# Kernel optimization log

Hardware: AMD Instinct MI355X
Metric: run time of the kernel (lower is better)

Reference implementation:

```python
import jax, jax.numpy as jnp
import numpy as np

D = 8       # q_dim / embed dim
NF = 8      # num_feats
OUT = 8     # out_dim


def _get_emb(sin_inp):
    # interleaved sin/cos, matching positional_encodings.get_emb
    return jnp.stack([jnp.sin(sin_inp), jnp.cos(sin_inp)], axis=-1).reshape(sin_inp.shape[0], -1)


def pos_encoding_2d(X, Y, ch, dtype=jnp.float32):
    # PositionalEncoding2D over dims (X=window, Y=num_feats), channels=ch
    c = int(np.ceil(ch / 4) * 2)
    inv_freq = jnp.asarray((1.0 / (10000.0 ** (np.arange(0, c, 2) / np.float32(c)))).astype(np.float32))
    emb_x = _get_emb(jnp.arange(X, dtype=dtype)[:, None] * inv_freq[None, :])  # (X, c)
    emb_y = _get_emb(jnp.arange(Y, dtype=dtype)[:, None] * inv_freq[None, :])  # (Y, c)
    emb = jnp.zeros((X, Y, 2 * c), dtype)
    emb = emb.at[:, :, :c].set(emb_x[:, None, :])
    emb = emb.at[:, :, c:2 * c].set(emb_y[None, :, :])
    return emb[:, :, :ch]


def layer_norm(x, g, b, eps=1e-5):
    mu = jnp.mean(x, axis=-1, keepdims=True)
    var = jnp.mean((x - mu) ** 2, axis=-1, keepdims=True)
    return (x - mu) * jax.lax.rsqrt(var + eps) * g + b


def setup_inputs() -> dict:
    key = jax.random.key(0)
    ks = jax.random.split(key, 12)
    B, W = 128, 2048
    x = jax.random.normal(ks[0], (B, W, NF), dtype=jnp.float32)
    m = jax.random.randint(ks[1], (B, W, NF), 0, 2, dtype=jnp.int32)
    m = m.at[:, :, 0].set(0)  # guarantee at least one unmasked key per row
    s = 0.1
    return {
        "x": x,
        "m": m,
        "emb_w": jax.random.normal(ks[2], (D, 1), jnp.float32) * s,
        "emb_b": jax.random.normal(ks[3], (D,), jnp.float32) * s,
        "emb_ln_g": jnp.ones((D,), jnp.float32),
        "emb_ln_b": jnp.zeros((D,), jnp.float32),
        "ln_g": jnp.ones((D,), jnp.float32),
        "ln_b": jnp.zeros((D,), jnp.float32),
        "var_query": jax.random.normal(ks[4], (1, 1, D), jnp.float32) * s,
        "in_proj_w": jax.random.normal(ks[5], (3 * D, D), jnp.float32) * s,
        "in_proj_b": jax.random.normal(ks[6], (3 * D,), jnp.float32) * s,
        "out_proj_w": jax.random.normal(ks[7], (D, D), jnp.float32) * s,
        "out_proj_b": jax.random.normal(ks[8], (D,), jnp.float32) * s,
        "proj_w": jax.random.normal(ks[9], (OUT, D), jnp.float32) * s,
        "proj_b": jax.random.normal(ks[10], (OUT,), jnp.float32) * s,
    }


def reference(x, m, emb_w, emb_b, emb_ln_g, emb_ln_b, ln_g, ln_b, var_query,
              in_proj_w, in_proj_b, out_proj_w, out_proj_b, proj_w, proj_b):
    B, W, F = x.shape
    d = emb_w.shape[0]
    # LinearEmbed: Linear(1, d) on each scalar, then LayerNorm(d)
    h = x[..., None] * emb_w[:, 0] + emb_b              # (B, W, F, d)
    h = layer_norm(h, emb_ln_g, emb_ln_b)
    # 2D positional encoding over (window, feature) dims
    h = h + pos_encoding_2d(W, F, d)[None]
    # pre-attention LayerNorm
    h = layer_norm(h, ln_g, ln_b)
    # single-query multihead (1 head) cross attention, key_padding_mask = m
    Wq, Wk, Wv = in_proj_w[:d], in_proj_w[d:2 * d], in_proj_w[2 * d:]
    bq, bk, bv = in_proj_b[:d], in_proj_b[d:2 * d], in_proj_b[2 * d:]
    qv = Wq @ var_query.reshape(d) + bq                 # (d,) shared query
    k = jnp.einsum('bwfd,ed->bwfe', h, Wk) + bk         # (B, W, F, d)
    v = jnp.einsum('bwfd,ed->bwfe', h, Wv) + bv         # (B, W, F, d)
    logits = jnp.einsum('bwfe,e->bwf', k, qv) / jnp.sqrt(jnp.float32(d))
    logits = jnp.where(m.astype(bool), -jnp.inf, logits)
    attn_w = jax.nn.softmax(logits, axis=-1)            # (B, W, F)
    attn = jnp.einsum('bwf,bwfe->bwe', attn_w, v)       # (B, W, d)
    attn = attn @ out_proj_w.T + out_proj_b
    # final projection
    out = attn @ proj_w.T + proj_b                      # (B, W, OUT)
    return out
```

## Files before the change

### kernel.cpp

```cpp
#include <hip/hip_runtime.h>
#include <math.h>

#define THREADS 256
#define W_DIM 2048
#define INV_SQRT8 0.35355339059327373f

__global__ __launch_bounds__(THREADS) void misstsm_fused(
    const float* __restrict__ x, const int* __restrict__ m,
    const float* __restrict__ emb_w, const float* __restrict__ emb_b,
    const float* __restrict__ emb_ln_g, const float* __restrict__ emb_ln_b,
    const float* __restrict__ ln_g, const float* __restrict__ ln_b,
    const float* __restrict__ var_query,
    const float* __restrict__ in_proj_w, const float* __restrict__ in_proj_b,
    const float* __restrict__ out_proj_w, const float* __restrict__ out_proj_b,
    const float* __restrict__ proj_w, const float* __restrict__ proj_b,
    float* __restrict__ out, int npos)
{
    __shared__ float s_M2[64];
    __shared__ float s_c2[8];
    __shared__ float s_a[8], s_bb[8], s_wlg[8];
    __shared__ float s_F[8][9];
    __shared__ float s_sc[12];

    const int t = threadIdx.x;
    const int half = npos >> 1;
    const int pos = blockIdx.x * THREADS + t;
    const int lp  = (pos < half) ? pos : (half - 1);

    const float4* xv4 = reinterpret_cast<const float4*>(x);
    const int4*   mv4 = reinterpret_cast<const int4*>(m);
    const float4 xa0 = xv4[lp*2+0],        xb0 = xv4[lp*2+1];
    const float4 xa1 = xv4[(lp+half)*2+0], xb1 = xv4[(lp+half)*2+1];
    const int4   ma0 = mv4[lp*2+0],        mb0 = mv4[lp*2+1];
    const int4   ma1 = mv4[(lp+half)*2+0], mb1 = mv4[(lp+half)*2+1];

    if (t < 64) {
        const int p = t >> 3, d = t & 7;
        float acc = 0.0f;
        #pragma unroll
        for (int e = 0; e < 8; ++e) {
            float po = 0.0f;
            #pragma unroll
            for (int o = 0; o < 8; ++o) po = fmaf(proj_w[p*8+o], out_proj_w[o*8+e], po);
            acc = fmaf(po, in_proj_w[(16+e)*8 + d], acc);
        }
        s_M2[t] = acc * ln_g[d];
    } else if (t < 72) {
        const int d = t - 64;
        float wk = 0.0f;
        #pragma unroll
        for (int e = 0; e < 8; ++e) {
            float qe = in_proj_b[e];
            #pragma unroll
            for (int dd = 0; dd < 8; ++dd) qe = fmaf(in_proj_w[e*8+dd], var_query[dd], qe);
            wk = fmaf(in_proj_w[(8+e)*8 + d], qe, wk);
        }
        s_wlg[d] = ln_g[d] * wk * INV_SQRT8;
    } else if (t < 80) {
        const int d = t - 72;
        float ewm = 0.0f, ebm = 0.0f;
        #pragma unroll
        for (int dd = 0; dd < 8; ++dd) { ewm += emb_w[dd]; ebm += emb_b[dd]; }
        ewm *= 0.125f; ebm *= 0.125f;
        s_a[d]  = (emb_w[d] - ewm) * emb_ln_g[d];
        s_bb[d] = (emb_b[d] - ebm) * emb_ln_g[d];
    } else if (t == 80) {
        float ewm = 0.0f, ebm = 0.0f;
        #pragma unroll
        for (int d = 0; d < 8; ++d) { ewm += emb_w[d]; ebm += emb_b[d]; }
        ewm *= 0.125f; ebm *= 0.125f;
        float A = 0.0f, Bc = 0.0f, Cc = 0.0f;
        #pragma unroll
        for (int d = 0; d < 8; ++d) {
            const float dw = emb_w[d] - ewm, db = emb_b[d] - ebm;
            A = fmaf(dw, dw, A); Bc = fmaf(dw, db, Bc); Cc = fmaf(db, db, Cc);
        }
        s_sc[0] = A * 0.125f;
        s_sc[1] = 2.0f * Bc * 0.125f;
        s_sc[2] = Cc * 0.125f + 1e-5f;
    } else if (t >= 128 && t < 136) {
        const int p = t - 128;
        float c = proj_b[p];
        #pragma unroll
        for (int o = 0; o < 8; ++o) {
            float ob2 = out_proj_b[o];
            #pragma unroll
            for (int e = 0; e < 8; ++e) ob2 = fmaf(out_proj_w[o*8+e], in_proj_b[16+e], ob2);
            c = fmaf(proj_w[p*8+o], ob2, c);
        }
        #pragma unroll
        for (int e = 0; e < 8; ++e) {
            float po = 0.0f;
            #pragma unroll
            for (int o = 0; o < 8; ++o) po = fmaf(proj_w[p*8+o], out_proj_w[o*8+e], po);
            #pragma unroll
            for (int d = 0; d < 8; ++d)
                c = fmaf(po * in_proj_w[(16+e)*8 + d], ln_b[d], c);
        }
        s_c2[p] = c;
    } else if (t == 136) {
        float qv[8]; float bkq = 0.0f;
        #pragma unroll
        for (int e = 0; e < 8; ++e) {
            float qe = in_proj_b[e];
            #pragma unroll
            for (int dd = 0; dd < 8; ++dd) qe = fmaf(in_proj_w[e*8+dd], var_query[dd], qe);
            qv[e] = qe;
            bkq = fmaf(in_proj_b[8+e], qe, bkq);
        }
        float ewm = 0.0f, ebm = 0.0f;
        #pragma unroll
        for (int d = 0; d < 8; ++d) { ewm += emb_w[d]; ebm += emb_b[d]; }
        ewm *= 0.125f; ebm *= 0.125f;
        float sa = 0, sb = 0, caa = 0, cbb = 0, cab = 0, ca = 0, cb = 0, sw = 0, ck = 0;
        #pragma unroll
        for (int d = 0; d < 8; ++d) {
            const float ad = (emb_w[d] - ewm) * emb_ln_g[d];
            const float bd = (emb_b[d] - ebm) * emb_ln_g[d];
            float wk = 0.0f;
            #pragma unroll
            for (int e = 0; e < 8; ++e) wk = fmaf(in_proj_w[(8+e)*8 + d], qv[e], wk);
            const float wl = ln_g[d] * wk * INV_SQRT8;
            sa += ad; sb += bd;
            caa = fmaf(ad, ad, caa); cbb = fmaf(bd, bd, cbb); cab = fmaf(ad, bd, cab);
            ca  = fmaf(ad, wl, ca);  cb  = fmaf(bd, wl, cb);
            sw += wl;
            ck  = fmaf(ln_b[d], wk, ck);
        }
        s_sc[3]  = sw;
        s_sc[4]  = (ck + bkq) * INV_SQRT8;
        s_sc[5]  = sa * 0.125f;
        s_sc[6]  = sb * 0.125f;
        s_sc[7]  = caa * 0.125f;
        s_sc[8]  = cbb * 0.125f;
        s_sc[9]  = cab * 0.25f;
        s_sc[10] = ca;
        s_sc[11] = cb;
    } else if (t >= 192 && t < 200) {
        const int f = t - 192;
        const float ff = (float)f;
        float sy0, cy0, sy1, cy1;
        sincosf(ff, &sy0, &cy0);
        sincosf(0.01f * ff, &sy1, &cy1);
        float Bf[4];
        Bf[0] = emb_ln_b[4] + sy0; Bf[1] = emb_ln_b[5] + cy0;
        Bf[2] = emb_ln_b[6] + sy1; Bf[3] = emb_ln_b[7] + cy1;
        float ewm = 0.0f, ebm = 0.0f;
        #pragma unroll
        for (int d = 0; d < 8; ++d) { ewm += emb_w[d]; ebm += emb_b[d]; }
        ewm *= 0.125f; ebm *= 0.125f;
        float qv[8];
        #pragma unroll
        for (int e = 0; e < 8; ++e) {
            float qe = in_proj_b[e];
            #pragma unroll
            for (int dd = 0; dd < 8; ++dd) qe = fmaf(in_proj_w[e*8+dd], var_query[dd], qe);
            qv[e] = qe;
        }
        float bsum = 0, aB = 0, bB = 0, b2 = 0, bdot = 0;
        #pragma unroll
        for (int j = 0; j < 4; ++j) {
            const int d = 4 + j;
            const float ad = (emb_w[d] - ewm) * emb_ln_g[d];
            const float bd = (emb_b[d] - ebm) * emb_ln_g[d];
            float wk = 0.0f;
            #pragma unroll
            for (int e = 0; e < 8; ++e) wk = fmaf(in_proj_w[(8+e)*8 + d], qv[e], wk);
            const float wl = ln_g[d] * wk * INV_SQRT8;
            bsum += Bf[j];
            aB   = fmaf(ad, Bf[j], aB);
            bB   = fmaf(bd, Bf[j], bB);
            b2   = fmaf(Bf[j], Bf[j], b2);
            bdot = fmaf(wl, Bf[j], bdot);
            s_F[f][j] = Bf[j];
        }
        s_F[f][4] = bsum * 0.125f;
        s_F[f][5] = aB * 0.25f;
        s_F[f][6] = bB * 0.25f;
        s_F[f][7] = b2 * 0.125f;
        s_F[f][8] = bdot;
    }
    __syncthreads();

    if (pos >= half) return;
    const int w = pos & (W_DIM - 1);

    const float A    = s_sc[0], twoB = s_sc[1], Cc  = s_sc[2];
    const float swlg = s_sc[3], cK   = s_sc[4];
    const float sa8  = s_sc[5], sb8  = s_sc[6];
    const float caa8 = s_sc[7], cbb8 = s_sc[8], cab8 = s_sc[9];
    const float ca   = s_sc[10], cb  = s_sc[11];

    const float fw = (float)w;
    float s1, c1, sl, clo;
    sincosf(fw, &s1, &c1);
    sincosf(0.01f * fw, &sl, &clo);
    float pB[4];
    pB[0] = emb_ln_b[0] + s1;  pB[1] = emb_ln_b[1] + c1;
    pB[2] = emb_ln_b[2] + sl;  pB[3] = emb_ln_b[3] + clo;

    float pBsum = 0, apB = 0, bpB = 0, pB2 = 0, pBdot = 0;
    #pragma unroll
    for (int j = 0; j < 4; ++j) {
        pBsum += pB[j];
        apB   = fmaf(s_a[j],   pB[j], apB);
        bpB   = fmaf(s_bb[j],  pB[j], bpB);
        pB2   = fmaf(pB[j],    pB[j], pB2);
        pBdot = fmaf(s_wlg[j], pB[j], pBdot);
    }
    const float pBsum8  = pBsum * 0.125f;
    const float twoapB8 = apB * 0.25f;
    const float twobpB8 = bpB * 0.25f;
    const float pB28eps = fmaf(pB2, 0.125f, 1e-5f);

    float4* ov4 = reinterpret_cast<float4*>(out);

    auto process = [&](const float4& Xa, const float4& Xb,
                       const int4& Ma, const int4& Mb, int opos) {
        const float xf[8] = {Xa.x, Xa.y, Xa.z, Xa.w, Xb.x, Xb.y, Xb.z, Xb.w};
        const int mk = (Ma.x!=0?1:0) | (Ma.y!=0?2:0) | (Ma.z!=0?4:0) | (Ma.w!=0?8:0)
                     | (Mb.x!=0?16:0) | (Mb.y!=0?32:0) | (Mb.z!=0?64:0) | (Mb.w!=0?128:0);

        float S = 0, SC = 0, ctt = 0, crr = 0, smu = 0;
        float avB[4] = {0, 0, 0, 0};

        #pragma unroll
        for (int f = 0; f < 8; ++f) {
            const float F0 = s_F[f][0], F1 = s_F[f][1], F2 = s_F[f][2], F3 = s_F[f][3];
            const float F4 = s_F[f][4], F5 = s_F[f][5], F6 = s_F[f][6], F7 = s_F[f][7];
            const float F8 = s_F[f][8];
            const float xs = xf[f];
            const float r  = rsqrtf(fmaf(xs, fmaf(xs, A, twoB), Cc));
            const float tt = xs * r;
            const float mu = fmaf(tt, sa8, fmaf(r, sb8, pBsum8 + F4));
            const float s2v = fmaf(tt, fmaf(tt, caa8, fmaf(r, cab8, twoapB8 + F5)),
                                   fmaf(r, fmaf(r, cbb8, twobpB8 + F6), pB28eps + F7));
            const float var = fmaf(-mu, mu, s2v);
            const float r2  = rsqrtf(var);
            const float dt  = fmaf(tt, ca, fmaf(r, cb, pBdot + F8));
            const float l   = fmaf(r2, fmaf(-mu, swlg, dt), cK);
            const float e   = __expf(l);
            const float pp  = ((mk >> f) & 1) ? 0.0f : e;
            const float cf  = pp * r2;
            S += pp; SC += cf;
            ctt = fmaf(cf, tt, ctt);
            crr = fmaf(cf, r,  crr);
            smu = fmaf(cf, mu, smu);
            avB[0] = fmaf(cf, F0, avB[0]);
            avB[1] = fmaf(cf, F1, avB[1]);
            avB[2] = fmaf(cf, F2, avB[2]);
            avB[3] = fmaf(cf, F3, avB[3]);
        }

        const float invS = 1.0f / S;
        const float nism = -invS * smu;
        float q[8];
        #pragma unroll
        for (int j = 0; j < 4; ++j) {
            const float av = fmaf(ctt, s_a[j], fmaf(crr, s_bb[j], SC * pB[j]));
            q[j] = fmaf(invS, av, nism);
        }
        #pragma unroll
        for (int j = 0; j < 4; ++j) {
            const float av = fmaf(ctt, s_a[4+j], fmaf(crr, s_bb[4+j], avB[j]));
            q[4+j] = fmaf(invS, av, nism);
        }

        float o[8];
        #pragma unroll
        for (int p = 0; p < 8; ++p) {
            float dp = s_c2[p];
            #pragma unroll
            for (int d = 0; d < 8; ++d) dp = fmaf(s_M2[p*8+d], q[d], dp);
            o[p] = dp;
        }
        ov4[opos*2+0] = make_float4(o[0], o[1], o[2], o[3]);
        ov4[opos*2+1] = make_float4(o[4], o[5], o[6], o[7]);
    };

    process(xa0, xb0, ma0, mb0, pos);
    process(xa1, xb1, ma1, mb1, pos + half);
}

extern "C" void kernel_launch(void* const* d_in, const int* in_sizes, int n_in,
                              void* d_out, int out_size, void* d_ws, size_t ws_size,
                              hipStream_t stream) {
    const float* x          = (const float*)d_in[0];
    const int*   m          = (const int*)d_in[1];
    const float* emb_w      = (const float*)d_in[2];
    const float* emb_b      = (const float*)d_in[3];
    const float* emb_ln_g   = (const float*)d_in[4];
    const float* emb_ln_b   = (const float*)d_in[5];
    const float* ln_g       = (const float*)d_in[6];
    const float* ln_b       = (const float*)d_in[7];
    const float* var_query  = (const float*)d_in[8];
    const float* in_proj_w  = (const float*)d_in[9];
    const float* in_proj_b  = (const float*)d_in[10];
    const float* out_proj_w = (const float*)d_in[11];
    const float* out_proj_b = (const float*)d_in[12];
    const float* proj_w     = (const float*)d_in[13];
    const float* proj_b     = (const float*)d_in[14];
    float* out = (float*)d_out;

    const int npos = in_sizes[0] / 8;
    const int half = npos >> 1;
    const int grid = (half + THREADS - 1) / THREADS;
    misstsm_fused<<<grid, THREADS, 0, stream>>>(
        x, m, emb_w, emb_b, emb_ln_g, emb_ln_b, ln_g, ln_b, var_query,
        in_proj_w, in_proj_b, out_proj_w, out_proj_b, proj_w, proj_b,
        out, npos);
}
```

Before: 14.00 us.

## Process one position per thread, fold log2e into logits, derive smu algebraically

```diff
diff --git a/kernel.cpp b/kernel.cpp
--- a/kernel.cpp
+++ b/kernel.cpp
@@ -4,6 +4,7 @@
 #define THREADS 256
 #define W_DIM 2048
 #define INV_SQRT8 0.35355339059327373f
+#define LOG2E 1.4426950408889634f
 
 __global__ __launch_bounds__(THREADS) void misstsm_fused(
     const float* __restrict__ x, const int* __restrict__ m,
@@ -23,16 +24,14 @@
     __shared__ float s_sc[12];
 
     const int t = threadIdx.x;
-    const int half = npos >> 1;
     const int pos = blockIdx.x * THREADS + t;
-    const int lp  = (pos < half) ? pos : (half - 1);
 
     const float4* xv4 = reinterpret_cast<const float4*>(x);
     const int4*   mv4 = reinterpret_cast<const int4*>(m);
-    const float4 xa0 = xv4[lp*2+0],        xb0 = xv4[lp*2+1];
-    const float4 xa1 = xv4[(lp+half)*2+0], xb1 = xv4[(lp+half)*2+1];
-    const int4   ma0 = mv4[lp*2+0],        mb0 = mv4[lp*2+1];
-    const int4   ma1 = mv4[(lp+half)*2+0], mb1 = mv4[(lp+half)*2+1];
+    const float4 xa = xv4[pos*2+0];
+    const float4 xb = xv4[pos*2+1];
+    const int4   ma = mv4[pos*2+0];
+    const int4   mb = mv4[pos*2+1];
 
     if (t < 64) {
         const int p = t >> 3, d = t & 7;
@@ -55,7 +54,7 @@
             for (int dd = 0; dd < 8; ++dd) qe = fmaf(in_proj_w[e*8+dd], var_query[dd], qe);
             wk = fmaf(in_proj_w[(8+e)*8 + d], qe, wk);
         }
-        s_wlg[d] = ln_g[d] * wk * INV_SQRT8;
+        s_wlg[d] = ln_g[d] * wk * (INV_SQRT8 * LOG2E);
     } else if (t < 80) {
         const int d = t - 72;
         float ewm = 0.0f, ebm = 0.0f;
@@ -120,7 +119,7 @@
             float wk = 0.0f;
             #pragma unroll
             for (int e = 0; e < 8; ++e) wk = fmaf(in_proj_w[(8+e)*8 + d], qv[e], wk);
-            const float wl = ln_g[d] * wk * INV_SQRT8;
+            const float wl = ln_g[d] * wk * (INV_SQRT8 * LOG2E);
             sa += ad; sb += bd;
             caa = fmaf(ad, ad, caa); cbb = fmaf(bd, bd, cbb); cab = fmaf(ad, bd, cab);
             ca  = fmaf(ad, wl, ca);  cb  = fmaf(bd, wl, cb);
@@ -128,7 +127,7 @@
             ck  = fmaf(ln_b[d], wk, ck);
         }
         s_sc[3]  = sw;
-        s_sc[4]  = (ck + bkq) * INV_SQRT8;
+        s_sc[4]  = (ck * LOG2E + bkq * LOG2E) * INV_SQRT8;
         s_sc[5]  = sa * 0.125f;
         s_sc[6]  = sb * 0.125f;
         s_sc[7]  = caa * 0.125f;
@@ -166,7 +165,7 @@
             float wk = 0.0f;
             #pragma unroll
             for (int e = 0; e < 8; ++e) wk = fmaf(in_proj_w[(8+e)*8 + d], qv[e], wk);
-            const float wl = ln_g[d] * wk * INV_SQRT8;
+            const float wl = ln_g[d] * wk * (INV_SQRT8 * LOG2E);
             bsum += Bf[j];
             aB   = fmaf(ad, Bf[j], aB);
             bB   = fmaf(bd, Bf[j], bB);
@@ -182,7 +181,6 @@
     }
     __syncthreads();
 
-    if (pos >= half) return;
     const int w = pos & (W_DIM - 1);
 
     const float A    = s_sc[0], twoB = s_sc[1], Cc  = s_sc[2];
@@ -213,73 +211,67 @@
     const float twobpB8 = bpB * 0.25f;
     const float pB28eps = fmaf(pB2, 0.125f, 1e-5f);
 
+    const float xf[8] = {xa.x, xa.y, xa.z, xa.w, xb.x, xb.y, xb.z, xb.w};
+    const int   mi[8] = {ma.x, ma.y, ma.z, ma.w, mb.x, mb.y, mb.z, mb.w};
+
+    float S = 0, SC = 0, ctt = 0, crr = 0;
+    float avB[4] = {0, 0, 0, 0};
+
+    #pragma unroll
+    for (int f = 0; f < 8; ++f) {
+        const float F0 = s_F[f][0], F1 = s_F[f][1], F2 = s_F[f][2], F3 = s_F[f][3];
+        const float F4 = s_F[f][4], F5 = s_F[f][5], F6 = s_F[f][6], F7 = s_F[f][7];
+        const float F8 = s_F[f][8];
+        const float xs = xf[f];
+        const float r  = rsqrtf(fmaf(xs, fmaf(xs, A, twoB), Cc));
+        const float tt = xs * r;
+        const float mu = fmaf(tt, sa8, fmaf(r, sb8, pBsum8 + F4));
+        const float s2v = fmaf(tt, fmaf(tt, caa8, fmaf(r, cab8, twoapB8 + F5)),
+                               fmaf(r, fmaf(r, cbb8, twobpB8 + F6), pB28eps + F7));
+        const float var = fmaf(-mu, mu, s2v);
+        const float r2  = rsqrtf(var);
+        const float dt  = fmaf(tt, ca, fmaf(r, cb, pBdot + F8));
+        const float l2  = fmaf(r2, fmaf(-mu, swlg, dt), cK);
+        const float e   = exp2f(l2);
+        const float pp  = mi[f] ? 0.0f : e;
+        const float cf  = pp * r2;
+        S += pp; SC += cf;
+        ctt = fmaf(cf, tt, ctt);
+        crr = fmaf(cf, r,  crr);
+        avB[0] = fmaf(cf, F0, avB[0]);
+        avB[1] = fmaf(cf, F1, avB[1]);
+        avB[2] = fmaf(cf, F2, avB[2]);
+        avB[3] = fmaf(cf, F3, avB[3]);
+    }
+
+    const float sumAvB = (avB[0] + avB[1]) + (avB[2] + avB[3]);
+    const float smu = fmaf(sa8, ctt, fmaf(sb8, crr, fmaf(pBsum8, SC, 0.125f * sumAvB)));
+
+    const float invS = 1.0f / S;
+    const float nism = -invS * smu;
+    float q[8];
+    #pragma unroll
+    for (int j = 0; j < 4; ++j) {
+        const float av = fmaf(ctt, s_a[j], fmaf(crr, s_bb[j], SC * pB[j]));
+        q[j] = fmaf(invS, av, nism);
+    }
+    #pragma unroll
+    for (int j = 0; j < 4; ++j) {
+        const float av = fmaf(ctt, s_a[4+j], fmaf(crr, s_bb[4+j], avB[j]));
+        q[4+j] = fmaf(invS, av, nism);
+    }
+
+    float o[8];
+    #pragma unroll
+    for (int p = 0; p < 8; ++p) {
+        float dp = s_c2[p];
+        #pragma unroll
+        for (int d = 0; d < 8; ++d) dp = fmaf(s_M2[p*8+d], q[d], dp);
+        o[p] = dp;
+    }
     float4* ov4 = reinterpret_cast<float4*>(out);
-
-    auto process = [&](const float4& Xa, const float4& Xb,
-                       const int4& Ma, const int4& Mb, int opos) {
-        const float xf[8] = {Xa.x, Xa.y, Xa.z, Xa.w, Xb.x, Xb.y, Xb.z, Xb.w};
-        const int mk = (Ma.x!=0?1:0) | (Ma.y!=0?2:0) | (Ma.z!=0?4:0) | (Ma.w!=0?8:0)
-                     | (Mb.x!=0?16:0) | (Mb.y!=0?32:0) | (Mb.z!=0?64:0) | (Mb.w!=0?128:0);
-
-        float S = 0, SC = 0, ctt = 0, crr = 0, smu = 0;
-        float avB[4] = {0, 0, 0, 0};
-
-        #pragma unroll
-        for (int f = 0; f < 8; ++f) {
-            const float F0 = s_F[f][0], F1 = s_F[f][1], F2 = s_F[f][2], F3 = s_F[f][3];
-            const float F4 = s_F[f][4], F5 = s_F[f][5], F6 = s_F[f][6], F7 = s_F[f][7];
-            const float F8 = s_F[f][8];
-            const float xs = xf[f];
-            const float r  = rsqrtf(fmaf(xs, fmaf(xs, A, twoB), Cc));
-            const float tt = xs * r;
-            const float mu = fmaf(tt, sa8, fmaf(r, sb8, pBsum8 + F4));
-            const float s2v = fmaf(tt, fmaf(tt, caa8, fmaf(r, cab8, twoapB8 + F5)),
-                                   fmaf(r, fmaf(r, cbb8, twobpB8 + F6), pB28eps + F7));
-            const float var = fmaf(-mu, mu, s2v);
-            const float r2  = rsqrtf(var);
-            const float dt  = fmaf(tt, ca, fmaf(r, cb, pBdot + F8));
-            const float l   = fmaf(r2, fmaf(-mu, swlg, dt), cK);
-            const float e   = __expf(l);
-            const float pp  = ((mk >> f) & 1) ? 0.0f : e;
-            const float cf  = pp * r2;
-            S += pp; SC += cf;
-            ctt = fmaf(cf, tt, ctt);
-            crr = fmaf(cf, r,  crr);
-            smu = fmaf(cf, mu, smu);
-            avB[0] = fmaf(cf, F0, avB[0]);
-            avB[1] = fmaf(cf, F1, avB[1]);
-            avB[2] = fmaf(cf, F2, avB[2]);
-            avB[3] = fmaf(cf, F3, avB[3]);
-        }
-
-        const float invS = 1.0f / S;
-        const float nism = -invS * smu;
-        float q[8];
-        #pragma unroll
-        for (int j = 0; j < 4; ++j) {
-            const float av = fmaf(ctt, s_a[j], fmaf(crr, s_bb[j], SC * pB[j]));
-            q[j] = fmaf(invS, av, nism);
-        }
-        #pragma unroll
-        for (int j = 0; j < 4; ++j) {
-            const float av = fmaf(ctt, s_a[4+j], fmaf(crr, s_bb[4+j], avB[j]));
-            q[4+j] = fmaf(invS, av, nism);
-        }
-
-        float o[8];
-        #pragma unroll
-        for (int p = 0; p < 8; ++p) {
-            float dp = s_c2[p];
-            #pragma unroll
-            for (int d = 0; d < 8; ++d) dp = fmaf(s_M2[p*8+d], q[d], dp);
-            o[p] = dp;
-        }
-        ov4[opos*2+0] = make_float4(o[0], o[1], o[2], o[3]);
-        ov4[opos*2+1] = make_float4(o[4], o[5], o[6], o[7]);
-    };
-
-    process(xa0, xb0, ma0, mb0, pos);
-    process(xa1, xb1, ma1, mb1, pos + half);
+    ov4[pos*2+0] = make_float4(o[0], o[1], o[2], o[3]);
+    ov4[pos*2+1] = make_float4(o[4], o[5], o[6], o[7]);
 }
 
 extern "C" void kernel_launch(void* const* d_in, const int* in_sizes, int n_in,
@@ -303,8 +295,7 @@
     float* out = (float*)d_out;
 
     const int npos = in_sizes[0] / 8;
-    const int half = npos >> 1;
-    const int grid = (half + THREADS - 1) / THREADS;
+    const int grid = (npos + THREADS - 1) / THREADS;
     misstsm_fused<<<grid, THREADS, 0, stream>>>(
         x, m, emb_w, emb_b, emb_ln_g, emb_ln_b, ln_g, ln_b, var_query,
         in_proj_w, in_proj_b, out_proj_w, out_proj_b, proj_w, proj_b,
```

Result: faster. 13.67 us (-2.3%).
